# Kernel optimization log

Measured on AMD Instinct MI355X. Metric: run time of the kernel, lower is better.

## Reference

```python
import jax, jax.numpy as jnp
import numpy as np

B, T, D, H = 2, 2048, 1024, 16


def setup_inputs() -> dict:
    key = jax.random.key(0)
    kx, kq, kk, kv, ko = jax.random.split(key, 5)
    s = D ** -0.5  # linear-layer init scale
    return {
        "x": jax.random.normal(kx, (B, T, D), dtype=jnp.float32),
        "Wq": jax.random.normal(kq, (D, D), dtype=jnp.float32) * s,
        "Wk": jax.random.normal(kk, (D, D), dtype=jnp.float32) * s,
        "Wv": jax.random.normal(kv, (D, D), dtype=jnp.float32) * s,
        "Wo": jax.random.normal(ko, (D, D), dtype=jnp.float32) * s,
        "quadrant_weights": jnp.array([1.0, -0.5, -0.5, 0.25], dtype=jnp.float32),
    }


def reference(x, Wq, Wk, Wv, Wo, quadrant_weights):
    Bx, Tx, Dx = x.shape
    d = Dx // H          # head dim
    h = d // 2           # quadrant (half-head) dim
    scale = h ** -0.5

    # projections -> (B, H, T, d)
    q = (x @ Wq).reshape(Bx, Tx, H, d).transpose(0, 2, 1, 3)
    k = (x @ Wk).reshape(Bx, Tx, H, d).transpose(0, 2, 1, 3)
    v = (x @ Wv).reshape(Bx, Tx, H, d).transpose(0, 2, 1, 3)

    q1, q2 = q[..., :h], q[..., h:]
    k1, k2 = k[..., :h], k[..., h:]

    w = jax.nn.softmax(quadrant_weights)
    # Fused quadrant sum: w0*q1k1^T + w1*q1k2^T + w2*q2k1^T + w3*q2k2^T
    # == q1 @ (w0*k1 + w1*k2)^T + q2 @ (w2*k1 + w3*k2)^T  (same math, fewer matmuls)
    k_eff1 = w[0] * k1 + w[1] * k2
    k_eff2 = w[2] * k1 + w[3] * k2
    attn = (jnp.einsum('bhqc,bhkc->bhqk', q1, k_eff1)
            + jnp.einsum('bhqc,bhkc->bhqk', q2, k_eff2)) * scale
    attn = jax.nn.softmax(attn, axis=-1)

    out = jnp.einsum('bhqk,bhkd->bhqd', attn, v)
    out = out.transpose(0, 2, 1, 3).reshape(Bx, Tx, Dx)
    return out @ Wo
```

## Files before the change

kernel.cpp:

```cpp
#include <hip/hip_runtime.h>

typedef unsigned short u16;
typedef unsigned int u32;
typedef __attribute__((ext_vector_type(8))) short short8;
typedef __attribute__((ext_vector_type(4))) short short4v;
typedef __attribute__((ext_vector_type(4))) float f32x4;
typedef __attribute__((ext_vector_type(16))) float f32x16;
typedef __attribute__((ext_vector_type(2))) unsigned u32x2;
typedef __attribute__((ext_vector_type(4))) unsigned u32x4;

__device__ __forceinline__ u16 f2bf(float f) {
  union { float f; unsigned u; } a; a.f = f;
  unsigned u = a.u + 0x7fffu + ((a.u >> 16) & 1u);
  return (u16)(u >> 16);
}
__device__ __forceinline__ u32 cvtpk(float lo, float hi_) {
  u32 r; asm("v_cvt_pk_bf16_f32 %0, %1, %2" : "=v"(r) : "v"(lo), "v"(hi_)); return r;
}
__device__ __forceinline__ void plswap(u32 &x, u32 &y) {
  asm("v_permlane32_swap_b32 %0, %1" : "+v"(x), "+v"(y));
}
__device__ __forceinline__ short8 as_short8(u32x4 v) {
  union { u32x4 u; short8 s; } c; c.u = v; return c.s;
}
__device__ __forceinline__ float fexp2(float x) {
  float r; asm("v_exp_f32 %0, %1" : "=v"(r) : "v"(x)); return r;
}
__device__ __forceinline__ void gload16(const u16* g, u16* l) {
  __builtin_amdgcn_global_load_lds(
      (__attribute__((address_space(1))) void*)(u16*)g,
      (__attribute__((address_space(3))) void*)l, 16, 0, 0);
}
__device__ __forceinline__ void keep8(short8 v) {
  union { short8 s; int i[4]; } u; u.s = v;
  asm volatile("" :: "v"(u.i[0]), "v"(u.i[1]), "v"(u.i[2]), "v"(u.i[3]));
}
__device__ __forceinline__ void wait_vm6() { asm volatile("s_waitcnt vmcnt(6)" ::: "memory"); }
__device__ __forceinline__ void wait_vm4() { asm volatile("s_waitcnt vmcnt(4)" ::: "memory"); }
__device__ __forceinline__ void wait_vm3() { asm volatile("s_waitcnt vmcnt(3)" ::: "memory"); }
__device__ __forceinline__ void wait_vm0() { asm volatile("s_waitcnt vmcnt(0)" ::: "memory"); }
__device__ __forceinline__ void barrier_raw() {
  __builtin_amdgcn_sched_barrier(0);
  __builtin_amdgcn_s_barrier();
  __builtin_amdgcn_sched_barrier(0);
}

__global__ void cvt_x_kernel(const float* __restrict__ x, u16* __restrict__ xb) {
  int i = (blockIdx.x * 256 + threadIdx.x) * 8;
  float4 a = *(const float4*)(x + i);
  float4 b = *(const float4*)(x + i + 4);
  short8 v;
  v[0] = (short)f2bf(a.x); v[1] = (short)f2bf(a.y);
  v[2] = (short)f2bf(a.z); v[3] = (short)f2bf(a.w);
  v[4] = (short)f2bf(b.x); v[5] = (short)f2bf(b.y);
  v[6] = (short)f2bf(b.z); v[7] = (short)f2bf(b.w);
  *(short8*)(xb + i) = v;
}

__global__ void prep_w_kernel(const float* __restrict__ Wq, const float* __restrict__ Wk,
                              const float* __restrict__ Wv, const float* __restrict__ Wo,
                              const float* __restrict__ qw,
                              u16* __restrict__ Wcat, u16* __restrict__ Wot) {
  __shared__ float tile[32][33];
  const int z = blockIdx.z;
  const int n0 = blockIdx.x * 32, k0 = blockIdx.y * 32;
  const float* src = (z == 0) ? Wq : (z == 1) ? Wk : (z == 2) ? Wv : Wo;
  float w0 = 0.f, w1 = 0.f, w2 = 0.f, w3 = 0.f;
  if (z == 1) {
    float a = qw[0], b = qw[1], c = qw[2], d = qw[3];
    float mx = fmaxf(fmaxf(a, b), fmaxf(c, d));
    float ea = expf(a - mx), eb = expf(b - mx), ec = expf(c - mx), ed = expf(d - mx);
    float s = ea + eb + ec + ed;
    w0 = ea / s; w1 = eb / s; w2 = ec / s; w3 = ed / s;
  }
  #pragma unroll
  for (int i = 0; i < 32; i += 8) {
    int k = k0 + threadIdx.y + i;
    int n = n0 + threadIdx.x;
    float v;
    if (z == 1) {
      int c = n & 63;
      if (c < 32) v = w0 * src[k * 1024 + n]      + w1 * src[k * 1024 + n + 32];
      else        v = w2 * src[k * 1024 + n - 32] + w3 * src[k * 1024 + n];
    } else {
      v = src[k * 1024 + n];
    }
    tile[threadIdx.y + i][threadIdx.x] = v;
  }
  __syncthreads();
  #pragma unroll
  for (int i = 0; i < 32; i += 8) {
    int n = n0 + threadIdx.y + i;
    int k = k0 + threadIdx.x;
    u16 v = f2bf(tile[threadIdx.x][threadIdx.y + i]);
    if (z < 3) Wcat[(size_t)(z * 1024 + n) * 1024 + k] = v;
    else       Wot[(size_t)n * 1024 + k] = v;
  }
}

template<int MODE, int BM>
__global__ __launch_bounds__(256, 2)
void gemm_k(const u16* __restrict__ A, const u16* __restrict__ Bm,
            u16* __restrict__ out_q, u16* __restrict__ out_k,
            u16* __restrict__ out_vt, float* __restrict__ out_f) {
  constexpr int WM = BM / 2;
  constexpr int MR = WM / 16;
  constexpr int RW = BM / 4;
  constexpr int NST = BM / 64 + 2;
  __shared__ u16 At[3][BM * 32];
  __shared__ u16 Bt[3][128 * 32];
  const int tid = threadIdx.x;
  const int wid = tid >> 6, lane = tid & 63;
  const int l15 = lane & 15, l4 = lane >> 4;

  const int nwg = gridDim.x * gridDim.y;
  const int cpx = nwg >> 3;
  int bid = blockIdx.y * gridDim.x + blockIdx.x;
  int wg = (bid & 7) * cpx + (bid >> 3);
  const int bx = wg % gridDim.x, by = wg / gridDim.x;
  const int mblk = by * BM, nblk = bx * 128;
  const int wm = (wid >> 1) * WM, wn = (wid & 1) * 64;
  f32x4 acc[MR][4] = {};

  const int rr = lane >> 2;
  const int cA = (lane & 3) * 8;
  const u16* gB = Bm + (size_t)(nblk + wid * 32 + rr) * 1024 + cA;
  const u16* gA = A + (size_t)(mblk + wid * RW + rr) * 1024 + cA;

  auto STAGE = [&](int ib, int kt) {
    #pragma unroll
    for (int q = 0; q < RW / 16; ++q)
      gload16(gA + (size_t)q * 16 * 1024 + kt, &At[ib][(wid * RW + q * 16) * 32]);
    #pragma unroll
    for (int q = 0; q < 2; ++q)
      gload16(gB + (size_t)q * 16 * 1024 + kt, &Bt[ib][(wid * 32 + q * 16) * 32]);
  };

  STAGE(0, 0);
  STAGE(1, 32);
  int ib = 0, ibw = 2;
  for (int s = 0; s < 32; ++s) {
    if (s < 31) {
      if constexpr (NST == 6) wait_vm6();
      else if constexpr (NST == 4) wait_vm4();
      else wait_vm3();
    } else wait_vm0();
    barrier_raw();
    if (s + 2 < 32) STAGE(ibw, (s + 2) * 32);
    short8 af[MR], bf[4];
    #pragma unroll
    for (int i = 0; i < MR; ++i)
      af[i] = *(const short8*)(&At[ib][(wm + i * 16 + l15) * 32 + l4 * 8]);
    #pragma unroll
    for (int j = 0; j < 4; ++j)
      bf[j] = *(const short8*)(&Bt[ib][(wn + j * 16 + l15) * 32 + l4 * 8]);
    #pragma unroll
    for (int i = 0; i < MR; ++i)
      #pragma unroll
      for (int j = 0; j < 4; ++j)
        acc[i][j] = __builtin_amdgcn_mfma_f32_16x16x32_bf16(af[i], bf[j], acc[i][j], 0, 0, 0);
    ib = (ib == 2) ? 0 : ib + 1;
    ibw = (ibw == 2) ? 0 : ibw + 1;
  }

  const float QSCALE = 0.17677669529663687f * 1.4426950408889634f;
  #pragma unroll
  for (int i = 0; i < MR; ++i) {
    int m_g = mblk + wm + i * 16 + l4 * 4;
    #pragma unroll
    for (int j = 0; j < 4; ++j) {
      int n_g = nblk + wn + j * 16 + l15;
      f32x4 v = acc[i][j];
      if (MODE == 1) {
        #pragma unroll
        for (int jj = 0; jj < 4; ++jj)
          out_f[(size_t)(m_g + jj) * 1024 + n_g] = v[jj];
      } else {
        if (n_g < 2048) {
          u16* dst; float sc;
          if (n_g < 1024) { dst = out_q; sc = QSCALE; } else { dst = out_k; sc = 1.0f; }
          int nn = n_g & 1023;
          #pragma unroll
          for (int jj = 0; jj < 4; ++jj)
            dst[(size_t)(m_g + jj) * 1024 + nn] = f2bf(v[jj] * sc);
        } else {
          int c = n_g - 2048;
          int b = m_g >> 11, t = m_g & 2047;
          short4v p;
          p[0] = (short)f2bf(v[0]); p[1] = (short)f2bf(v[1]);
          p[2] = (short)f2bf(v[2]); p[3] = (short)f2bf(v[3]);
          *(short4v*)(out_vt + ((size_t)((b << 4) + (c >> 6)) * 64 + (c & 63)) * 2048 + t) = p;
        }
      }
    }
  }
}

__global__ __launch_bounds__(256)
void attn_k(const u16* __restrict__ Q, const u16* __restrict__ Kb,
            const u16* __restrict__ Vt, u16* __restrict__ O) {
  __shared__ u16 lk[3][64 * 64];
  __shared__ u16 lv[3][64 * 64];
  const int tid = threadIdx.x, wid = tid >> 6, lane = tid & 63;
  const int l31 = lane & 31, hi = lane >> 5;

  int bid = blockIdx.y * 16 + blockIdx.x;
  int wg = (bid & 7) * 64 + (bid >> 3);
  const int qt = wg & 15, bh = wg >> 4;
  const int b = bh >> 4, h = bh & 15;
  const int qrow = qt * 128 + wid * 32 + l31;

  short8 qf[4];
  #pragma unroll
  for (int cs = 0; cs < 4; ++cs)
    qf[cs] = *(const short8*)(Q + (size_t)(b * 2048 + qrow) * 1024 + h * 64 + cs * 16 + hi * 8);
  #pragma unroll
  for (int cs = 0; cs < 4; ++cs) keep8(qf[cs]);

  const int sr = lane >> 3;
  const int sc8 = (lane & 7) ^ sr;
  const u16* Kg = Kb + (size_t)b * 2048 * 1024 + h * 64 + sc8 * 8;
  const u16* Vg = Vt + (size_t)bh * 64 * 2048 + sc8 * 8;
  const int s0i = wid * 2;
  const int swz = l31 & 7;

  short8 onesf;
  #pragma unroll
  for (int j = 0; j < 8; ++j) onesf[j] = (short)0x3F80;
  const f32x16 z16 = {};

  f32x16 accO0 = {}, accO1 = {}, sacc = {};

  auto STAGE = [&](int tt, int ibx) {
    #pragma unroll
    for (int s2 = 0; s2 < 2; ++s2) {
      int s = s0i + s2;
      int r = s * 8 + sr;
      gload16(Kg + (size_t)(tt * 64 + r) * 1024, &lk[ibx][s * 512]);
      gload16(Vg + (size_t)r * 2048 + tt * 64, &lv[ibx][s * 512]);
    }
  };

  STAGE(0, 0);
  STAGE(1, 1);
  int ib = 0, ibw = 2;

  for (int t = 0; t < 32; ++t) {
    if (t < 31) wait_vm4(); else wait_vm0();
    barrier_raw();
    if (t + 2 < 32) STAGE(t + 2, ibw);

    const u16* kb = lk[ib];
    const u16* vb = lv[ib];

    f32x16 s0v, s1v;
    __builtin_amdgcn_s_setprio(1);
    {
      short8 k0 = *(const short8*)(kb + l31 * 64 + ((hi ^ swz) * 8));
      short8 k1 = *(const short8*)(kb + (32 + l31) * 64 + ((hi ^ swz) * 8));
      s0v = __builtin_amdgcn_mfma_f32_32x32x16_bf16(k0, qf[0], z16, 0, 0, 0);
      s1v = __builtin_amdgcn_mfma_f32_32x32x16_bf16(k1, qf[0], z16, 0, 0, 0);
    }
    #pragma unroll
    for (int cs = 1; cs < 4; ++cs) {
      int ch = cs * 2 + hi;
      short8 k0 = *(const short8*)(kb + l31 * 64 + ((ch ^ swz) * 8));
      short8 k1 = *(const short8*)(kb + (32 + l31) * 64 + ((ch ^ swz) * 8));
      s0v = __builtin_amdgcn_mfma_f32_32x32x16_bf16(k0, qf[cs], s0v, 0, 0, 0);
      s1v = __builtin_amdgcn_mfma_f32_32x32x16_bf16(k1, qf[cs], s1v, 0, 0, 0);
    }
    __builtin_amdgcn_s_setprio(0);

    #pragma unroll
    for (int i = 0; i < 16; ++i) { s0v[i] = fexp2(s0v[i]); s1v[i] = fexp2(s1v[i]); }

    short8 paS[4];
    #pragma unroll
    for (int half = 0; half < 2; ++half) {
      #pragma unroll
      for (int kq = 0; kq < 2; ++kq) {
        float p0, p1, p2, p3, p4, p5, p6, p7;
        if (half == 0) {
          p0 = s0v[kq*8+0]; p1 = s0v[kq*8+1]; p2 = s0v[kq*8+2]; p3 = s0v[kq*8+3];
          p4 = s0v[kq*8+4]; p5 = s0v[kq*8+5]; p6 = s0v[kq*8+6]; p7 = s0v[kq*8+7];
        } else {
          p0 = s1v[kq*8+0]; p1 = s1v[kq*8+1]; p2 = s1v[kq*8+2]; p3 = s1v[kq*8+3];
          p4 = s1v[kq*8+4]; p5 = s1v[kq*8+5]; p6 = s1v[kq*8+6]; p7 = s1v[kq*8+7];
        }
        u32 A = cvtpk(p0, p1), B = cvtpk(p2, p3);
        u32 C = cvtpk(p4, p5), D = cvtpk(p6, p7);
        plswap(A, C);
        plswap(B, D);
        u32x4 w; w[0] = A; w[1] = B; w[2] = C; w[3] = D;
        paS[half * 2 + kq] = as_short8(w);
      }
    }

    __builtin_amdgcn_s_setprio(1);
    #pragma unroll
    for (int ks = 0; ks < 4; ++ks) {
      int ch = ks * 2 + hi;
      short8 v0 = *(const short8*)(vb + l31 * 64 + ((ch ^ swz) * 8));
      short8 v1 = *(const short8*)(vb + (32 + l31) * 64 + ((ch ^ swz) * 8));
      accO0 = __builtin_amdgcn_mfma_f32_32x32x16_bf16(v0, paS[ks], accO0, 0, 0, 0);
      accO1 = __builtin_amdgcn_mfma_f32_32x32x16_bf16(v1, paS[ks], accO1, 0, 0, 0);
      sacc  = __builtin_amdgcn_mfma_f32_32x32x16_bf16(onesf, paS[ks], sacc, 0, 0, 0);
    }
    __builtin_amdgcn_s_setprio(0);

    ib = (ib == 2) ? 0 : ib + 1;
    ibw = (ibw == 2) ? 0 : ibw + 1;
  }

  float inv = 1.0f / sacc[0];
  u16* Op = O + (size_t)(b * 2048 + qrow) * 1024 + h * 64;
  #pragma unroll
  for (int g = 0; g < 4; ++g) {
    u32x2 pr;
    pr[0] = cvtpk(accO0[4*g] * inv, accO0[4*g+1] * inv);
    pr[1] = cvtpk(accO0[4*g+2] * inv, accO0[4*g+3] * inv);
    *(u32x2*)(Op + 8*g + 4*hi) = pr;
    u32x2 pr2;
    pr2[0] = cvtpk(accO1[4*g] * inv, accO1[4*g+1] * inv);
    pr2[1] = cvtpk(accO1[4*g+2] * inv, accO1[4*g+3] * inv);
    *(u32x2*)(Op + 32 + 8*g + 4*hi) = pr2;
  }
}

extern "C" void kernel_launch(void* const* d_in, const int* in_sizes, int n_in,
                              void* d_out, int out_size, void* d_ws, size_t ws_size,
                              hipStream_t stream) {
  const float* x  = (const float*)d_in[0];
  const float* Wq = (const float*)d_in[1];
  const float* Wk = (const float*)d_in[2];
  const float* Wv = (const float*)d_in[3];
  const float* Wo = (const float*)d_in[4];
  const float* qw = (const float*)d_in[5];

  char* w = (char*)d_ws;
  u16* xb   = (u16*)(w);
  u16* Wcat = (u16*)(w + (8u  << 20));
  u16* Wot  = (u16*)(w + (14u << 20));
  u16* Qb   = (u16*)(w + (16u << 20));
  u16* Kb   = (u16*)(w + (24u << 20));
  u16* Vtb  = (u16*)(w + (32u << 20));
  u16* Ob   = (u16*)(w + (40u << 20));

  cvt_x_kernel<<<2048, 256, 0, stream>>>(x, xb);
  prep_w_kernel<<<dim3(32, 32, 4), dim3(32, 8), 0, stream>>>(Wq, Wk, Wv, Wo, qw, Wcat, Wot);
  gemm_k<0, 256><<<dim3(24, 16), 256, 0, stream>>>(xb, Wcat, Qb, Kb, Vtb, nullptr);
  attn_k<<<dim3(16, 32), 256, 0, stream>>>(Qb, Kb, Vtb, Ob);
  gemm_k<1, 64><<<dim3(8, 64), 256, 0, stream>>>(Ob, Wot, nullptr, nullptr, nullptr, (float*)d_out);
}
```

Before: 132.4 us.

## Split attention over key halves with a merge pass, shrink QKV GEMM tile

The attention kernel now splits the key sequence into two halves, doubling the grid to 1024 blocks. Each block writes an unnormalized bf16 partial output plus its row sum, and a new merge kernel combines the two halves and normalizes. The attention pipeline drops from three LDS buffers to two with a full vmcnt(0) wait each step, and launch bounds request 4 blocks per CU. The QKV GEMM uses 128-row tiles for twice the blocks. This trades more parallelism and occupancy for an extra kernel launch, extra partial-output traffic, and bf16 rounding of the partials before the merge.

Result: faster. 122.0 us (-7.8%).

```diff
diff --git a/kernel.cpp b/kernel.cpp
--- a/kernel.cpp
+++ b/kernel.cpp
@@ -14,6 +14,10 @@
   unsigned u = a.u + 0x7fffu + ((a.u >> 16) & 1u);
   return (u16)(u >> 16);
 }
+__device__ __forceinline__ float bf2f(short s) {
+  union { unsigned u; float f; } a; a.u = ((unsigned)(unsigned short)s) << 16;
+  return a.f;
+}
 __device__ __forceinline__ u32 cvtpk(float lo, float hi_) {
   u32 r; asm("v_cvt_pk_bf16_f32 %0, %1, %2" : "=v"(r) : "v"(lo), "v"(hi_)); return r;
 }
@@ -35,7 +39,6 @@
   union { short8 s; int i[4]; } u; u.s = v;
   asm volatile("" :: "v"(u.i[0]), "v"(u.i[1]), "v"(u.i[2]), "v"(u.i[3]));
 }
-__device__ __forceinline__ void wait_vm6() { asm volatile("s_waitcnt vmcnt(6)" ::: "memory"); }
 __device__ __forceinline__ void wait_vm4() { asm volatile("s_waitcnt vmcnt(4)" ::: "memory"); }
 __device__ __forceinline__ void wait_vm3() { asm volatile("s_waitcnt vmcnt(3)" ::: "memory"); }
 __device__ __forceinline__ void wait_vm0() { asm volatile("s_waitcnt vmcnt(0)" ::: "memory"); }
@@ -141,8 +144,7 @@
   int ib = 0, ibw = 2;
   for (int s = 0; s < 32; ++s) {
     if (s < 31) {
-      if constexpr (NST == 6) wait_vm6();
-      else if constexpr (NST == 4) wait_vm4();
+      if constexpr (NST == 4) wait_vm4();
       else wait_vm3();
     } else wait_vm0();
     barrier_raw();
@@ -196,17 +198,20 @@
   }
 }
 
-__global__ __launch_bounds__(256)
+__global__ __launch_bounds__(256, 4)
 void attn_k(const u16* __restrict__ Q, const u16* __restrict__ Kb,
-            const u16* __restrict__ Vt, u16* __restrict__ O) {
-  __shared__ u16 lk[3][64 * 64];
-  __shared__ u16 lv[3][64 * 64];
+            const u16* __restrict__ Vt, u16* __restrict__ Opart,
+            float* __restrict__ L) {
+  __shared__ u16 lk[2][64 * 64];
+  __shared__ u16 lv[2][64 * 64];
   const int tid = threadIdx.x, wid = tid >> 6, lane = tid & 63;
   const int l31 = lane & 31, hi = lane >> 5;
 
   int bid = blockIdx.y * 16 + blockIdx.x;
-  int wg = (bid & 7) * 64 + (bid >> 3);
-  const int qt = wg & 15, bh = wg >> 4;
+  int wg = (bid & 7) * 128 + (bid >> 3);
+  const int qt = wg & 15;
+  const int yy = wg >> 4;
+  const int half = yy & 1, bh = yy >> 1;
   const int b = bh >> 4, h = bh & 15;
   const int qrow = qt * 128 + wid * 32 + l31;
 
@@ -219,8 +224,8 @@
 
   const int sr = lane >> 3;
   const int sc8 = (lane & 7) ^ sr;
-  const u16* Kg = Kb + (size_t)b * 2048 * 1024 + h * 64 + sc8 * 8;
-  const u16* Vg = Vt + (size_t)bh * 64 * 2048 + sc8 * 8;
+  const u16* Kg = Kb + ((size_t)b * 2048 + half * 1024) * 1024 + h * 64 + sc8 * 8;
+  const u16* Vg = Vt + (size_t)bh * 64 * 2048 + half * 1024 + sc8 * 8;
   const int s0i = wid * 2;
   const int swz = l31 & 7;
 
@@ -242,16 +247,14 @@
   };
 
   STAGE(0, 0);
-  STAGE(1, 1);
-  int ib = 0, ibw = 2;
-
-  for (int t = 0; t < 32; ++t) {
-    if (t < 31) wait_vm4(); else wait_vm0();
+
+  for (int t = 0; t < 16; ++t) {
+    wait_vm0();
     barrier_raw();
-    if (t + 2 < 32) STAGE(t + 2, ibw);
-
-    const u16* kb = lk[ib];
-    const u16* vb = lv[ib];
+    if (t + 1 < 16) STAGE(t + 1, (t + 1) & 1);
+
+    const u16* kb = lk[t & 1];
+    const u16* vb = lv[t & 1];
 
     f32x16 s0v, s1v;
     __builtin_amdgcn_s_setprio(1);
@@ -276,11 +279,11 @@
 
     short8 paS[4];
     #pragma unroll
-    for (int half = 0; half < 2; ++half) {
+    for (int hf = 0; hf < 2; ++hf) {
       #pragma unroll
       for (int kq = 0; kq < 2; ++kq) {
         float p0, p1, p2, p3, p4, p5, p6, p7;
-        if (half == 0) {
+        if (hf == 0) {
           p0 = s0v[kq*8+0]; p1 = s0v[kq*8+1]; p2 = s0v[kq*8+2]; p3 = s0v[kq*8+3];
           p4 = s0v[kq*8+4]; p5 = s0v[kq*8+5]; p6 = s0v[kq*8+6]; p7 = s0v[kq*8+7];
         } else {
@@ -292,7 +295,7 @@
         plswap(A, C);
         plswap(B, D);
         u32x4 w; w[0] = A; w[1] = B; w[2] = C; w[3] = D;
-        paS[half * 2 + kq] = as_short8(w);
+        paS[hf * 2 + kq] = as_short8(w);
       }
     }
 
@@ -307,24 +310,48 @@
       sacc  = __builtin_amdgcn_mfma_f32_32x32x16_bf16(onesf, paS[ks], sacc, 0, 0, 0);
     }
     __builtin_amdgcn_s_setprio(0);
-
-    ib = (ib == 2) ? 0 : ib + 1;
-    ibw = (ibw == 2) ? 0 : ibw + 1;
-  }
-
-  float inv = 1.0f / sacc[0];
-  u16* Op = O + (size_t)(b * 2048 + qrow) * 1024 + h * 64;
+  }
+
+  u16* Po = Opart + (size_t)(half * 4096 + b * 2048 + qrow) * 1024 + h * 64;
   #pragma unroll
   for (int g = 0; g < 4; ++g) {
     u32x2 pr;
-    pr[0] = cvtpk(accO0[4*g] * inv, accO0[4*g+1] * inv);
-    pr[1] = cvtpk(accO0[4*g+2] * inv, accO0[4*g+3] * inv);
-    *(u32x2*)(Op + 8*g + 4*hi) = pr;
+    pr[0] = cvtpk(accO0[4*g],    accO0[4*g+1]);
+    pr[1] = cvtpk(accO0[4*g+2],  accO0[4*g+3]);
+    *(u32x2*)(Po + 8*g + 4*hi) = pr;
     u32x2 pr2;
-    pr2[0] = cvtpk(accO1[4*g] * inv, accO1[4*g+1] * inv);
-    pr2[1] = cvtpk(accO1[4*g+2] * inv, accO1[4*g+3] * inv);
-    *(u32x2*)(Op + 32 + 8*g + 4*hi) = pr2;
-  }
+    pr2[0] = cvtpk(accO1[4*g],   accO1[4*g+1]);
+    pr2[1] = cvtpk(accO1[4*g+2], accO1[4*g+3]);
+    *(u32x2*)(Po + 32 + 8*g + 4*hi) = pr2;
+  }
+  if (hi == 0)
+    L[(size_t)(half * 32 + bh) * 2048 + qrow] = sacc[0];
+}
+
+__global__ __launch_bounds__(256)
+void merge_k(const u16* __restrict__ Opart, const float* __restrict__ L,
+             u16* __restrict__ Ob) {
+  int i = blockIdx.x * 256 + threadIdx.x;
+  int e = i * 8;
+  int row = e >> 10;
+  int col = e & 1023;
+  int h = col >> 6;
+  int b = row >> 11;
+  int tr = row & 2047;
+  int bh = b * 16 + h;
+  float l1 = L[(size_t)bh * 2048 + tr];
+  float l2 = L[(size_t)(32 + bh) * 2048 + tr];
+  float inv = 1.0f / (l1 + l2);
+  short8 o1 = *(const short8*)(Opart + (size_t)row * 1024 + col);
+  short8 o2 = *(const short8*)(Opart + (size_t)(4096 + row) * 1024 + col);
+  u32x4 w;
+  #pragma unroll
+  for (int j = 0; j < 4; ++j) {
+    float lo = (bf2f(o1[2*j])   + bf2f(o2[2*j]))   * inv;
+    float hi_ = (bf2f(o1[2*j+1]) + bf2f(o2[2*j+1])) * inv;
+    w[j] = cvtpk(lo, hi_);
+  }
+  *(u32x4*)(Ob + (size_t)row * 1024 + col) = w;
 }
 
 extern "C" void kernel_launch(void* const* d_in, const int* in_sizes, int n_in,
@@ -338,17 +365,20 @@
   const float* qw = (const float*)d_in[5];
 
   char* w = (char*)d_ws;
-  u16* xb   = (u16*)(w);
-  u16* Wcat = (u16*)(w + (8u  << 20));
-  u16* Wot  = (u16*)(w + (14u << 20));
-  u16* Qb   = (u16*)(w + (16u << 20));
-  u16* Kb   = (u16*)(w + (24u << 20));
-  u16* Vtb  = (u16*)(w + (32u << 20));
-  u16* Ob   = (u16*)(w + (40u << 20));
+  u16* Wot   = (u16*)(w);
+  u16* Qb    = (u16*)(w + (2u  << 20));
+  u16* Kb    = (u16*)(w + (10u << 20));
+  u16* Vtb   = (u16*)(w + (18u << 20));
+  u16* xb    = (u16*)(w + (26u << 20));
+  u16* Wcat  = (u16*)(w + (34u << 20));
+  u16* Opart = (u16*)(w + (26u << 20));
+  float* L   = (float*)(w + (42u << 20));
+  u16* Ob    = Qb;
 
   cvt_x_kernel<<<2048, 256, 0, stream>>>(x, xb);
   prep_w_kernel<<<dim3(32, 32, 4), dim3(32, 8), 0, stream>>>(Wq, Wk, Wv, Wo, qw, Wcat, Wot);
-  gemm_k<0, 256><<<dim3(24, 16), 256, 0, stream>>>(xb, Wcat, Qb, Kb, Vtb, nullptr);
-  attn_k<<<dim3(16, 32), 256, 0, stream>>>(Qb, Kb, Vtb, Ob);
+  gemm_k<0, 128><<<dim3(24, 32), 256, 0, stream>>>(xb, Wcat, Qb, Kb, Vtb, nullptr);
+  attn_k<<<dim3(16, 64), 256, 0, stream>>>(Qb, Kb, Vtb, Opart, L);
+  merge_k<<<2048, 256, 0, stream>>>(Opart, L, Ob);
   gemm_k<1, 64><<<dim3(8, 64), 256, 0, stream>>>(Ob, Wot, nullptr, nullptr, nullptr, (float*)d_out);
 }
```
